# Kernel tuning notes

Measured on AMD Instinct MI355X. Metric: run time of the kernel, lower is better.

Reference implementation:

```python
import jax, jax.numpy as jnp
import numpy as np

N_NODES = 50000

def _gcn_layer(x, src, dst, W, b, n_nodes):
    # Linear transform first (PyG GCNConv): h = x @ W
    h = x @ W  # [N, out]
    # Add self-loops
    loop = jnp.arange(n_nodes, dtype=src.dtype)
    src2 = jnp.concatenate([src, loop])
    dst2 = jnp.concatenate([dst, loop])
    # Symmetric normalization deg^-1/2 (deg counts incoming edges incl. self-loop)
    deg = jax.ops.segment_sum(jnp.ones_like(dst2, dtype=h.dtype), dst2, num_segments=n_nodes)
    dinv = jnp.where(deg > 0, jax.lax.rsqrt(deg), 0.0)
    norm = dinv[src2] * dinv[dst2]  # [E+N]
    # Gather-scale-scatter aggregation
    msg = h[src2] * norm[:, None]  # [E+N, out]
    out = jax.ops.segment_sum(msg, dst2, num_segments=n_nodes)
    return out + b

def setup_inputs() -> dict:
    key = jax.random.key(0)
    k1, k2, k3, k4 = jax.random.split(key, 4)
    E = 800000
    x = jax.random.normal(k1, (N_NODES, 128), dtype=jnp.float32)
    edge_index = jax.random.randint(k2, (2, E), 0, N_NODES, dtype=jnp.int64)
    W1 = jax.random.normal(k3, (128, 512), dtype=jnp.float32) * (1.0 / np.sqrt(128))
    b1 = jnp.zeros((512,), dtype=jnp.float32)
    W2 = jax.random.normal(k4, (512, 250), dtype=jnp.float32) * (1.0 / np.sqrt(512))
    b2 = jnp.zeros((250,), dtype=jnp.float32)
    return {"x": x, "edge_index": edge_index, "W1": W1, "b1": b1, "W2": W2, "b2": b2}

def reference(x, edge_index, W1, b1, W2, b2):
    src, dst = edge_index[0], edge_index[1]
    h = _gcn_layer(x, src, dst, W1, b1, N_NODES)
    h = jax.nn.relu(h)
    h = _gcn_layer(h, src, dst, W2, b2, N_NODES)
    return jax.nn.relu(h)
```

## Files before the change

### kernel.cpp

```cpp
#include <hip/hip_runtime.h>

#define N_NODES 50000

typedef __attribute__((ext_vector_type(8))) short bf16x8;
typedef __attribute__((ext_vector_type(4))) float f32x4;

__device__ __forceinline__ ushort f2bf(float f) {
    union { float f; unsigned u; } v; v.f = f;
    unsigned r = v.u + 0x7fff + ((v.u >> 16) & 1);
    return (ushort)(r >> 16);
}
__device__ __forceinline__ float bf2f(ushort u) {
    union { unsigned u; float f; } v; v.u = ((unsigned)u) << 16;
    return v.f;
}
__device__ __forceinline__ float bf2f_lo(unsigned u) {
    union { unsigned u; float f; } v; v.u = u << 16;
    return v.f;
}
__device__ __forceinline__ float bf2f_hi(unsigned u) {
    union { unsigned u; float f; } v; v.u = u & 0xffff0000u;
    return v.f;
}

__device__ __forceinline__ int eload(const void* ei, int idx, int is64) {
    return is64 ? (int)((const long long*)ei)[idx] : ((const int*)ei)[idx];
}

__global__ void k_init(const void* ei, int* flag, int* deg, int n) {
    if (blockIdx.x == 0) {
        __shared__ int bad;
        if (threadIdx.x == 0) bad = 0;
        __syncthreads();
        long long v = ((const long long*)ei)[threadIdx.x];
        if (v < 0 || v >= N_NODES) atomicOr(&bad, 1);
        __syncthreads();
        if (threadIdx.x == 0) *flag = bad ? 0 : 1;
    }
    int i = blockIdx.x * 256 + threadIdx.x;
    if (i < n) deg[i] = 0;
}

__global__ void k_hist(const void* ei, const int* flag, int* deg, int e) {
    int base = (blockIdx.x * blockDim.x + threadIdx.x) * 4;
    if (base >= e) return;
    int is64 = *flag;
    if (base + 4 <= e) {
        int d0 = eload(ei, e + base,     is64);
        int d1 = eload(ei, e + base + 1, is64);
        int d2 = eload(ei, e + base + 2, is64);
        int d3 = eload(ei, e + base + 3, is64);
        atomicAdd(&deg[d0], 1);
        atomicAdd(&deg[d1], 1);
        atomicAdd(&deg[d2], 1);
        atomicAdd(&deg[d3], 1);
    } else {
        for (int i = base; i < e; ++i)
            atomicAdd(&deg[eload(ei, e + i, is64)], 1);
    }
}

__global__ __launch_bounds__(512)
void k_scanA(const int* __restrict__ deg, int* __restrict__ rp1,
             int* __restrict__ bsum, int n) {
    __shared__ int wsum[8];
    const int i = blockIdx.x * 512 + threadIdx.x;
    const int lane = threadIdx.x & 63, wid = threadIdx.x >> 6;
    int x = (i < n) ? deg[i] : 0;
    #pragma unroll
    for (int off = 1; off < 64; off <<= 1) {
        int y = __shfl_up(x, off, 64);
        if (lane >= off) x += y;
    }
    if (lane == 63) wsum[wid] = x;
    __syncthreads();
    if (wid == 0 && lane < 8) {
        int s = wsum[lane];
        #pragma unroll
        for (int off = 1; off < 8; off <<= 1) {
            int y = __shfl_up(s, off, 64);
            if (lane >= off) s += y;
        }
        wsum[lane] = s;
    }
    __syncthreads();
    int incl = x + (wid > 0 ? wsum[wid - 1] : 0);
    if (i < n) rp1[i] = incl;
    if (threadIdx.x == 0) bsum[blockIdx.x] = wsum[7];
}

__global__ __launch_bounds__(512)
void k_scanC(const int* __restrict__ deg, int* __restrict__ rowptr,
             const int* __restrict__ bsum, int* __restrict__ cur,
             float* __restrict__ dinv, int n, int nb) {
    __shared__ int spart[2];
    if (threadIdx.x < 128) {
        int v = (threadIdx.x < nb && (int)threadIdx.x < (int)blockIdx.x)
                ? bsum[threadIdx.x] : 0;
        #pragma unroll
        for (int o = 32; o; o >>= 1) v += __shfl_down(v, o, 64);
        if ((threadIdx.x & 63) == 0) spart[threadIdx.x >> 6] = v;
    }
    __syncthreads();
    const int off = spart[0] + spart[1];
    const int i = blockIdx.x * 512 + threadIdx.x;
    if (i >= n) return;
    const int d = deg[i];
    const int incl = rowptr[i + 1] + off;
    rowptr[i + 1] = incl;
    cur[i] = incl - d;
    dinv[i] = rsqrtf((float)(d + 1));
    if (i == 0) rowptr[0] = 0;
}

__global__ void k_fill(const void* ei, const int* flag, int* cur, int* adj, int e) {
    const int phase = blockIdx.x & 7;
    const int lo = phase * (N_NODES / 8);
    const int hi = lo + (N_NODES / 8);
    const int i = (blockIdx.x >> 3) * 256 + threadIdx.x;
    if (i >= e) return;
    const int is64 = *flag;
    const int d = eload(ei, e + i, is64);
    if (d >= lo && d < hi) {
        const int s = eload(ei, i, is64);
        adj[atomicAdd(&cur[d], 1)] = s;
    }
}

__global__ void k_splitW(const float* __restrict__ W1, const float* __restrict__ W2,
                         ushort* __restrict__ o1, ushort* __restrict__ o2) {
    int idx = blockIdx.x * 256 + threadIdx.x;
    if (idx < 512 * 128) {
        int nn = idx >> 7, k = idx & 127;
        o1[idx] = f2bf(W1[(size_t)k * 512 + nn]);
    } else {
        idx -= 512 * 128;
        int nn = idx >> 9, k = idx & 511;
        o2[idx] = (nn < 250) ? f2bf(W2[(size_t)k * 250 + nn]) : (ushort)0;
    }
}

__global__ __launch_bounds__(256)
void k_scale(const float* __restrict__ x, const float* __restrict__ dinv,
             ushort* __restrict__ xs, int n) {
    int idx = blockIdx.x * 256 + threadIdx.x;
    if (idx >= n * 64) return;
    int i = idx >> 6;
    float2 v = ((const float2*)x)[idx];
    float d = dinv[i];
    ((unsigned*)xs)[idx] = (unsigned)f2bf(d * v.x) | ((unsigned)f2bf(d * v.y) << 16);
}

__global__ __launch_bounds__(256)
void k_pull128b(const int* __restrict__ rowptr, const int* __restrict__ adj,
                const float* __restrict__ dinv, const ushort* __restrict__ xs,
                ushort* __restrict__ ohi, int n) {
    const int i = blockIdx.x * 4 + (threadIdx.x >> 6);
    if (i >= n) return;
    const int lane = threadIdx.x & 63;
    const unsigned* xs32 = (const unsigned*)xs;
    unsigned u = xs32[(size_t)i * 64 + lane];
    float a0 = bf2f_lo(u), a1 = bf2f_hi(u);
    int j = rowptr[i];
    const int end = rowptr[i + 1];
    for (; j + 8 <= end; j += 8) {
        int s0 = adj[j],     s1 = adj[j + 1], s2 = adj[j + 2], s3 = adj[j + 3];
        int s4 = adj[j + 4], s5 = adj[j + 5], s6 = adj[j + 6], s7 = adj[j + 7];
        unsigned u0 = xs32[(size_t)s0 * 64 + lane];
        unsigned u1 = xs32[(size_t)s1 * 64 + lane];
        unsigned u2 = xs32[(size_t)s2 * 64 + lane];
        unsigned u3 = xs32[(size_t)s3 * 64 + lane];
        unsigned u4 = xs32[(size_t)s4 * 64 + lane];
        unsigned u5 = xs32[(size_t)s5 * 64 + lane];
        unsigned u6 = xs32[(size_t)s6 * 64 + lane];
        unsigned u7 = xs32[(size_t)s7 * 64 + lane];
        a0 += bf2f_lo(u0) + bf2f_lo(u1) + bf2f_lo(u2) + bf2f_lo(u3);
        a1 += bf2f_hi(u0) + bf2f_hi(u1) + bf2f_hi(u2) + bf2f_hi(u3);
        a0 += bf2f_lo(u4) + bf2f_lo(u5) + bf2f_lo(u6) + bf2f_lo(u7);
        a1 += bf2f_hi(u4) + bf2f_hi(u5) + bf2f_hi(u6) + bf2f_hi(u7);
    }
    for (; j + 4 <= end; j += 4) {
        int s0 = adj[j], s1 = adj[j + 1], s2 = adj[j + 2], s3 = adj[j + 3];
        unsigned u0 = xs32[(size_t)s0 * 64 + lane];
        unsigned u1 = xs32[(size_t)s1 * 64 + lane];
        unsigned u2 = xs32[(size_t)s2 * 64 + lane];
        unsigned u3 = xs32[(size_t)s3 * 64 + lane];
        a0 += bf2f_lo(u0) + bf2f_lo(u1) + bf2f_lo(u2) + bf2f_lo(u3);
        a1 += bf2f_hi(u0) + bf2f_hi(u1) + bf2f_hi(u2) + bf2f_hi(u3);
    }
    for (; j < end; ++j) {
        unsigned us = xs32[(size_t)adj[j] * 64 + lane];
        a0 += bf2f_lo(us);
        a1 += bf2f_hi(us);
    }
    const float di = dinv[i];
    a0 *= di; a1 *= di;
    ((unsigned*)ohi)[(size_t)i * 64 + lane] =
        (unsigned)f2bf(a0) | ((unsigned)f2bf(a1) << 16);
}

__global__ __launch_bounds__(256)
void k_pull250v(const int* __restrict__ rowptr, const int* __restrict__ adj,
                const float* __restrict__ dinv, const ushort* __restrict__ t,
                const float* __restrict__ bias, float* __restrict__ out, int n) {
    const int i = blockIdx.x * 4 + (threadIdx.x >> 6);
    if (i >= n) return;
    const int lane = threadIdx.x & 63;
    const uint2* t2 = (const uint2*)t;
    uint2 u = t2[(size_t)i * 64 + lane];
    float a0 = bf2f_lo(u.x), a1 = bf2f_hi(u.x);
    float a2 = bf2f_lo(u.y), a3 = bf2f_hi(u.y);
    int j = rowptr[i];
    const int end = rowptr[i + 1];
    for (; j + 8 <= end; j += 8) {
        int s0 = adj[j],     s1 = adj[j + 1], s2 = adj[j + 2], s3 = adj[j + 3];
        int s4 = adj[j + 4], s5 = adj[j + 5], s6 = adj[j + 6], s7 = adj[j + 7];
        uint2 u0 = t2[(size_t)s0 * 64 + lane];
        uint2 u1 = t2[(size_t)s1 * 64 + lane];
        uint2 u2 = t2[(size_t)s2 * 64 + lane];
        uint2 u3 = t2[(size_t)s3 * 64 + lane];
        uint2 u4 = t2[(size_t)s4 * 64 + lane];
        uint2 u5 = t2[(size_t)s5 * 64 + lane];
        uint2 u6 = t2[(size_t)s6 * 64 + lane];
        uint2 u7 = t2[(size_t)s7 * 64 + lane];
        a0 += bf2f_lo(u0.x) + bf2f_lo(u1.x) + bf2f_lo(u2.x) + bf2f_lo(u3.x);
        a1 += bf2f_hi(u0.x) + bf2f_hi(u1.x) + bf2f_hi(u2.x) + bf2f_hi(u3.x);
        a2 += bf2f_lo(u0.y) + bf2f_lo(u1.y) + bf2f_lo(u2.y) + bf2f_lo(u3.y);
        a3 += bf2f_hi(u0.y) + bf2f_hi(u1.y) + bf2f_hi(u2.y) + bf2f_hi(u3.y);
        a0 += bf2f_lo(u4.x) + bf2f_lo(u5.x) + bf2f_lo(u6.x) + bf2f_lo(u7.x);
        a1 += bf2f_hi(u4.x) + bf2f_hi(u5.x) + bf2f_hi(u6.x) + bf2f_hi(u7.x);
        a2 += bf2f_lo(u4.y) + bf2f_lo(u5.y) + bf2f_lo(u6.y) + bf2f_lo(u7.y);
        a3 += bf2f_hi(u4.y) + bf2f_hi(u5.y) + bf2f_hi(u6.y) + bf2f_hi(u7.y);
    }
    for (; j + 4 <= end; j += 4) {
        int s0 = adj[j], s1 = adj[j + 1], s2 = adj[j + 2], s3 = adj[j + 3];
        uint2 u0 = t2[(size_t)s0 * 64 + lane];
        uint2 u1 = t2[(size_t)s1 * 64 + lane];
        uint2 u2 = t2[(size_t)s2 * 64 + lane];
        uint2 u3 = t2[(size_t)s3 * 64 + lane];
        a0 += bf2f_lo(u0.x) + bf2f_lo(u1.x) + bf2f_lo(u2.x) + bf2f_lo(u3.x);
        a1 += bf2f_hi(u0.x) + bf2f_hi(u1.x) + bf2f_hi(u2.x) + bf2f_hi(u3.x);
        a2 += bf2f_lo(u0.y) + bf2f_lo(u1.y) + bf2f_lo(u2.y) + bf2f_lo(u3.y);
        a3 += bf2f_hi(u0.y) + bf2f_hi(u1.y) + bf2f_hi(u2.y) + bf2f_hi(u3.y);
    }
    for (; j < end; ++j) {
        uint2 us = t2[(size_t)adj[j] * 64 + lane];
        a0 += bf2f_lo(us.x); a1 += bf2f_hi(us.x);
        a2 += bf2f_lo(us.y); a3 += bf2f_hi(us.y);
    }
    const float d = dinv[i];
    const int c0 = lane * 4;
    if (lane < 62) {
        float2 b0 = *(const float2*)&bias[c0];
        float2 b1 = *(const float2*)&bias[c0 + 2];
        float2 o0, o1;
        o0.x = fmaxf(d * a0 + b0.x, 0.0f);
        o0.y = fmaxf(d * a1 + b0.y, 0.0f);
        o1.x = fmaxf(d * a2 + b1.x, 0.0f);
        o1.y = fmaxf(d * a3 + b1.y, 0.0f);
        *(float2*)&out[(size_t)i * 250 + c0] = o0;
        *(float2*)&out[(size_t)i * 250 + c0 + 2] = o1;
    } else if (lane == 62) {
        float2 b0 = *(const float2*)&bias[248];
        float2 o0;
        o0.x = fmaxf(d * a0 + b0.x, 0.0f);
        o0.y = fmaxf(d * a1 + b0.y, 0.0f);
        *(float2*)&out[(size_t)i * 250 + 248] = o0;
    }
}

__device__ __forceinline__ void gl16(const ushort* g, ushort* l) {
    __builtin_amdgcn_global_load_lds((const __attribute__((address_space(1))) void*)g,
                                     (__attribute__((address_space(3))) void*)l,
                                     16, 0, 0);
}

#define OFF_B 4096
#define SMEM_HALF 12288

__global__ __launch_bounds__(256, 2)
void k_mfma(const ushort* __restrict__ A, const ushort* __restrict__ B,
            const float* __restrict__ bias, const float* __restrict__ rscale,
            ushort* __restrict__ outp, int M, int K, int ldc, int mode,
            int CX, int PY) {
    __shared__ __align__(16) ushort smem[2 * SMEM_HALF];

    int id = blockIdx.x;
    const int gsz = CX * 8;
    const int nfull = (PY >> 3) * gsz;
    int bx, by;
    if (id < nfull) {
        int gg = id / gsz;
        int r  = id - gg * gsz;
        bx = r >> 3;
        by = gg * 8 + (r & 7);
    } else {
        int rem  = id - nfull;
        int pbase = (PY >> 3) << 3;
        int prem  = PY - pbase;
        by = pbase + rem % prem;
        bx = rem / prem;
    }
    const int brow = by * 128;
    const int bcol = bx * 256;

    const int tid  = threadIdx.x;
    const int lane = tid & 63;
    const int w    = tid >> 6;
    const int g    = lane >> 4;
    const int lr   = lane & 15;

    auto STAGE = [&](ushort* buf, int k0) {
        const int kofs = k0 + w * 8;
        #pragma unroll
        for (int t2 = 0; t2 < 2; ++t2)
            gl16(A + (size_t)(brow + t2 * 64 + lane) * K + kofs,
                 buf + w * 1024 + t2 * 512);
        #pragma unroll
        for (int t4 = 0; t4 < 4; ++t4)
            gl16(B + (size_t)(bcol + t4 * 64 + lane) * K + kofs,
                 buf + OFF_B + w * 2048 + t4 * 512);
    };

    f32x4 acc[8][4] = {};

    auto COMPUTE = [&](const ushort* rb) {
        bf16x8 af[8], bh[4];
        #pragma unroll
        for (int nt = 0; nt < 4; ++nt)
            bh[nt] = *(const bf16x8*)(rb + OFF_B + g * 2048 + (w * 64 + nt * 16 + lr) * 8);
        #pragma unroll
        for (int mt = 0; mt < 8; ++mt)
            af[mt] = *(const bf16x8*)(rb + g * 1024 + (mt * 16 + lr) * 8);
        #pragma unroll
        for (int mt = 0; mt < 8; ++mt)
            #pragma unroll
            for (int nt = 0; nt < 4; ++nt)
                acc[mt][nt] = __builtin_amdgcn_mfma_f32_16x16x32_bf16(bh[nt], af[mt], acc[mt][nt], 0, 0, 0);
    };

    STAGE(smem, 0);
    int cur = 0;
    for (int k0 = 32; k0 < K; k0 += 32) {
        STAGE(smem + (cur ^ 1) * SMEM_HALF, k0);
        asm volatile("s_waitcnt vmcnt(6)" ::: "memory");
        __builtin_amdgcn_sched_barrier(0);
        __builtin_amdgcn_s_barrier();
        COMPUTE(smem + cur * SMEM_HALF);
        __builtin_amdgcn_sched_barrier(0);
        __builtin_amdgcn_s_barrier();
        cur ^= 1;
    }
    asm volatile("s_waitcnt vmcnt(0)" ::: "memory");
    __builtin_amdgcn_sched_barrier(0);
    __builtin_amdgcn_s_barrier();
    COMPUTE(smem + cur * SMEM_HALF);

    #pragma unroll
    for (int mt = 0; mt < 8; ++mt) {
        const int gr = brow + mt * 16 + lr;
        if (gr >= M) continue;
        const float rs = (mode == 0) ? rscale[gr] : 0.0f;
        #pragma unroll
        for (int nt = 0; nt < 4; ++nt) {
            const int gc0 = bcol + w * 64 + nt * 16 + g * 4;
            float v0, v1, v2, v3;
            if (mode == 0) {
                v0 = acc[mt][nt][0] * rs; v1 = acc[mt][nt][1] * rs;
                v2 = acc[mt][nt][2] * rs; v3 = acc[mt][nt][3] * rs;
            } else {
                const float4 bv = *(const float4*)&bias[gc0];
                v0 = fmaxf(acc[mt][nt][0] + bv.x, 0.0f);
                v1 = fmaxf(acc[mt][nt][1] + bv.y, 0.0f);
                v2 = fmaxf(acc[mt][nt][2] + bv.z, 0.0f);
                v3 = fmaxf(acc[mt][nt][3] + bv.w, 0.0f);
            }
            uint2 pk;
            pk.x = (unsigned)f2bf(v0) | ((unsigned)f2bf(v1) << 16);
            pk.y = (unsigned)f2bf(v2) | ((unsigned)f2bf(v3) << 16);
            *(uint2*)(outp + (size_t)gr * ldc + gc0) = pk;
        }
    }
}

extern "C" void kernel_launch(void* const* d_in, const int* in_sizes, int n_in,
                              void* d_out, int out_size, void* d_ws, size_t ws_size,
                              hipStream_t stream) {
    const float* x  = (const float*)d_in[0];
    const void*  ei = d_in[1];
    const float* W1 = (const float*)d_in[2];
    const float* b1 = (const float*)d_in[3];
    const float* W2 = (const float*)d_in[4];
    const float* b2 = (const float*)d_in[5];
    float* out = (float*)d_out;

    const int N = N_NODES;
    const int E = in_sizes[1] / 2;
    const int MPAD = 50048;
    const int NSCB = (N + 511) / 512;

    char* base = (char*)d_ws;
    int*   flag   = (int*)base;
    int*   deg    = (int*)(base + 256);
    int*   rowptr = deg + 51200;
    int*   cur    = rowptr + 51200;
    float* dinv   = (float*)(cur + 51200);
    int*   bsum   = (int*)(dinv + 51200);
    int*   adj    = bsum + 128;
    char*  p      = (char*)(adj + ((E + 63) & ~63));
    ushort* A1hi  = (ushort*)p;  p += (size_t)MPAD * 128 * 2;
    ushort* A1xx  = (ushort*)p;  p += (size_t)MPAD * 128 * 2;
    ushort* tbuf  = A1hi;
    ushort* h1hi  = (ushort*)p;  p += (size_t)MPAD * 512 * 2;
    ushort* Bt1   = (ushort*)p;  p += 512 * 128 * 2;
    ushort* Bt2   = (ushort*)p;  p += 256 * 512 * 2;
    ushort* xs    = (ushort*)p;  p += (size_t)MPAD * 128 * 2;
    (void)A1xx;

    k_init<<<(N + 255) / 256, 256, 0, stream>>>(ei, flag, deg, N);
    k_hist<<<(E / 4 + 255) / 256, 256, 0, stream>>>(ei, flag, deg, E);
    k_scanA<<<NSCB, 512, 0, stream>>>(deg, rowptr + 1, bsum, N);
    k_scanC<<<NSCB, 512, 0, stream>>>(deg, rowptr, bsum, cur, dinv, N, NSCB);
    k_fill<<<((E + 255) / 256) * 8, 256, 0, stream>>>(ei, flag, cur, adj, E);

    k_splitW<<<(512 * 128 + 256 * 512) / 256, 256, 0, stream>>>(W1, W2, Bt1, Bt2);
    k_scale<<<(N * 64 + 255) / 256, 256, 0, stream>>>(x, dinv, xs, N);

    k_pull128b<<<(N + 3) / 4, 256, 0, stream>>>(rowptr, adj, dinv, xs, A1hi, N);

    k_mfma<<<2 * 391, 256, 0, stream>>>(A1hi, Bt1, b1, nullptr, h1hi,
                                        N, 128, 512, 1, 2, 391);

    k_mfma<<<1 * 391, 256, 0, stream>>>(h1hi, Bt2, nullptr, dinv, tbuf,
                                        N, 512, 256, 0, 1, 391);

    k_pull250v<<<(N + 3) / 4, 256, 0, stream>>>(rowptr, adj, dinv, tbuf, b2, out, N);
}
```

Before: 264.4 us.

## Add dedicated single-shot K=128 GEMM kernel and fold weight conversion into init

Measured after the change: 264.8 us. About the same (+0.2%).

```diff
diff --git a/kernel.cpp b/kernel.cpp
--- a/kernel.cpp
+++ b/kernel.cpp
@@ -27,7 +27,9 @@
     return is64 ? (int)((const long long*)ei)[idx] : ((const int*)ei)[idx];
 }
 
-__global__ void k_init(const void* ei, int* flag, int* deg, int n) {
+__global__ void k_init(const void* ei, int* flag, int* deg, int n,
+                       const float* __restrict__ W1, const float* __restrict__ W2,
+                       ushort* __restrict__ o1, ushort* __restrict__ o2) {
     if (blockIdx.x == 0) {
         __shared__ int bad;
         if (threadIdx.x == 0) bad = 0;
@@ -39,6 +41,14 @@
     }
     int i = blockIdx.x * 256 + threadIdx.x;
     if (i < n) deg[i] = 0;
+    if (i < 512 * 128) {
+        int nn = i >> 7, k = i & 127;
+        o1[i] = f2bf(W1[(size_t)k * 512 + nn]);
+    } else if (i < 512 * 128 + 256 * 512) {
+        int idx = i - 512 * 128;
+        int nn = idx >> 9, k = idx & 511;
+        o2[idx] = (nn < 250) ? f2bf(W2[(size_t)k * 250 + nn]) : (ushort)0;
+    }
 }
 
 __global__ void k_hist(const void* ei, const int* flag, int* deg, int e) {
@@ -124,19 +134,6 @@
     if (d >= lo && d < hi) {
         const int s = eload(ei, i, is64);
         adj[atomicAdd(&cur[d], 1)] = s;
-    }
-}
-
-__global__ void k_splitW(const float* __restrict__ W1, const float* __restrict__ W2,
-                         ushort* __restrict__ o1, ushort* __restrict__ o2) {
-    int idx = blockIdx.x * 256 + threadIdx.x;
-    if (idx < 512 * 128) {
-        int nn = idx >> 7, k = idx & 127;
-        o1[idx] = f2bf(W1[(size_t)k * 512 + nn]);
-    } else {
-        idx -= 512 * 128;
-        int nn = idx >> 9, k = idx & 511;
-        o2[idx] = (nn < 250) ? f2bf(W2[(size_t)k * 250 + nn]) : (ushort)0;
     }
 }
 
@@ -275,15 +272,13 @@
                                      16, 0, 0);
 }
 
-#define OFF_B 4096
-#define SMEM_HALF 12288
+#define G1_OFFB 16384
 
 __global__ __launch_bounds__(256, 2)
-void k_mfma(const ushort* __restrict__ A, const ushort* __restrict__ B,
-            const float* __restrict__ bias, const float* __restrict__ rscale,
-            ushort* __restrict__ outp, int M, int K, int ldc, int mode,
-            int CX, int PY) {
-    __shared__ __align__(16) ushort smem[2 * SMEM_HALF];
+void k_mfma1(const ushort* __restrict__ A, const ushort* __restrict__ B,
+             const float* __restrict__ bias, ushort* __restrict__ outp,
+             int M, int CX, int PY) {
+    __shared__ __align__(16) ushort smem[32768];
 
     int id = blockIdx.x;
     const int gsz = CX * 8;
@@ -302,11 +297,94 @@
         bx = rem / prem;
     }
     const int brow = by * 128;
+    const int bcol = bx * 128;
+
+    const int lane = threadIdx.x & 63;
+    const int w    = threadIdx.x >> 6;
+    const int g    = lane >> 4;
+    const int lr   = lane & 15;
+    const int wm   = w >> 1, wn = w & 1;
+
+    #pragma unroll
+    for (int t = 0; t < 8; ++t) {
+        const int idx = w * 8 + t;
+        const int c  = idx >> 1;
+        const int r0 = (idx & 1) * 64;
+        const int doff = c * 1024 + r0 * 8;
+        gl16(A + (size_t)(brow + r0 + lane) * 128 + c * 8, smem + doff);
+        gl16(B + (size_t)(bcol + r0 + lane) * 128 + c * 8, smem + G1_OFFB + doff);
+    }
+    asm volatile("s_waitcnt vmcnt(0)" ::: "memory");
+    __builtin_amdgcn_sched_barrier(0);
+    __builtin_amdgcn_s_barrier();
+
+    f32x4 acc[4][4] = {};
+    #pragma unroll
+    for (int ks = 0; ks < 4; ++ks) {
+        bf16x8 af[4], bh[4];
+        const int cb = (ks * 4 + g) * 1024;
+        #pragma unroll
+        for (int i = 0; i < 4; ++i) {
+            af[i] = *(const bf16x8*)(smem + cb + (wm * 64 + i * 16 + lr) * 8);
+            bh[i] = *(const bf16x8*)(smem + G1_OFFB + cb + (wn * 64 + i * 16 + lr) * 8);
+        }
+        #pragma unroll
+        for (int mt = 0; mt < 4; ++mt)
+            #pragma unroll
+            for (int nt = 0; nt < 4; ++nt)
+                acc[mt][nt] = __builtin_amdgcn_mfma_f32_16x16x32_bf16(bh[nt], af[mt], acc[mt][nt], 0, 0, 0);
+    }
+
+    #pragma unroll
+    for (int mt = 0; mt < 4; ++mt) {
+        const int gr = brow + wm * 64 + mt * 16 + lr;
+        if (gr >= M) continue;
+        #pragma unroll
+        for (int nt = 0; nt < 4; ++nt) {
+            const int gc0 = bcol + wn * 64 + nt * 16 + g * 4;
+            const float4 bv = *(const float4*)&bias[gc0];
+            float v0 = fmaxf(acc[mt][nt][0] + bv.x, 0.0f);
+            float v1 = fmaxf(acc[mt][nt][1] + bv.y, 0.0f);
+            float v2 = fmaxf(acc[mt][nt][2] + bv.z, 0.0f);
+            float v3 = fmaxf(acc[mt][nt][3] + bv.w, 0.0f);
+            uint2 pk;
+            pk.x = (unsigned)f2bf(v0) | ((unsigned)f2bf(v1) << 16);
+            pk.y = (unsigned)f2bf(v2) | ((unsigned)f2bf(v3) << 16);
+            *(uint2*)(outp + (size_t)gr * 512 + gc0) = pk;
+        }
+    }
+}
+
+#define OFF_B 4096
+#define SMEM_HALF 12288
+
+__global__ __launch_bounds__(256, 2)
+void k_mfma(const ushort* __restrict__ A, const ushort* __restrict__ B,
+            const float* __restrict__ rscale, ushort* __restrict__ outp,
+            int M, int K, int ldc, int CX, int PY) {
+    __shared__ __align__(16) ushort smem[2 * SMEM_HALF];
+
+    int id = blockIdx.x;
+    const int gsz = CX * 8;
+    const int nfull = (PY >> 3) * gsz;
+    int bx, by;
+    if (id < nfull) {
+        int gg = id / gsz;
+        int r  = id - gg * gsz;
+        bx = r >> 3;
+        by = gg * 8 + (r & 7);
+    } else {
+        int rem  = id - nfull;
+        int pbase = (PY >> 3) << 3;
+        int prem  = PY - pbase;
+        by = pbase + rem % prem;
+        bx = rem / prem;
+    }
+    const int brow = by * 128;
     const int bcol = bx * 256;
 
-    const int tid  = threadIdx.x;
-    const int lane = tid & 63;
-    const int w    = tid >> 6;
+    const int lane = threadIdx.x & 63;
+    const int w    = threadIdx.x >> 6;
     const int g    = lane >> 4;
     const int lr   = lane & 15;
 
@@ -360,24 +438,15 @@
     for (int mt = 0; mt < 8; ++mt) {
         const int gr = brow + mt * 16 + lr;
         if (gr >= M) continue;
-        const float rs = (mode == 0) ? rscale[gr] : 0.0f;
+        const float rs = rscale[gr];
         #pragma unroll
         for (int nt = 0; nt < 4; ++nt) {
             const int gc0 = bcol + w * 64 + nt * 16 + g * 4;
-            float v0, v1, v2, v3;
-            if (mode == 0) {
-                v0 = acc[mt][nt][0] * rs; v1 = acc[mt][nt][1] * rs;
-                v2 = acc[mt][nt][2] * rs; v3 = acc[mt][nt][3] * rs;
-            } else {
-                const float4 bv = *(const float4*)&bias[gc0];
-                v0 = fmaxf(acc[mt][nt][0] + bv.x, 0.0f);
-                v1 = fmaxf(acc[mt][nt][1] + bv.y, 0.0f);
-                v2 = fmaxf(acc[mt][nt][2] + bv.z, 0.0f);
-                v3 = fmaxf(acc[mt][nt][3] + bv.w, 0.0f);
-            }
             uint2 pk;
-            pk.x = (unsigned)f2bf(v0) | ((unsigned)f2bf(v1) << 16);
-            pk.y = (unsigned)f2bf(v2) | ((unsigned)f2bf(v3) << 16);
+            pk.x = (unsigned)f2bf(acc[mt][nt][0] * rs) |
+                   ((unsigned)f2bf(acc[mt][nt][1] * rs) << 16);
+            pk.y = (unsigned)f2bf(acc[mt][nt][2] * rs) |
+                   ((unsigned)f2bf(acc[mt][nt][3] * rs) << 16);
             *(uint2*)(outp + (size_t)gr * ldc + gc0) = pk;
         }
     }
@@ -417,22 +486,20 @@
     ushort* xs    = (ushort*)p;  p += (size_t)MPAD * 128 * 2;
     (void)A1xx;
 
-    k_init<<<(N + 255) / 256, 256, 0, stream>>>(ei, flag, deg, N);
+    const int initBlocks = (512 * 128 + 256 * 512 + 255) / 256;
+    k_init<<<initBlocks, 256, 0, stream>>>(ei, flag, deg, N, W1, W2, Bt1, Bt2);
     k_hist<<<(E / 4 + 255) / 256, 256, 0, stream>>>(ei, flag, deg, E);
     k_scanA<<<NSCB, 512, 0, stream>>>(deg, rowptr + 1, bsum, N);
     k_scanC<<<NSCB, 512, 0, stream>>>(deg, rowptr, bsum, cur, dinv, N, NSCB);
     k_fill<<<((E + 255) / 256) * 8, 256, 0, stream>>>(ei, flag, cur, adj, E);
 
-    k_splitW<<<(512 * 128 + 256 * 512) / 256, 256, 0, stream>>>(W1, W2, Bt1, Bt2);
     k_scale<<<(N * 64 + 255) / 256, 256, 0, stream>>>(x, dinv, xs, N);
 
     k_pull128b<<<(N + 3) / 4, 256, 0, stream>>>(rowptr, adj, dinv, xs, A1hi, N);
 
-    k_mfma<<<2 * 391, 256, 0, stream>>>(A1hi, Bt1, b1, nullptr, h1hi,
-                                        N, 128, 512, 1, 2, 391);
-
-    k_mfma<<<1 * 391, 256, 0, stream>>>(h1hi, Bt2, nullptr, dinv, tbuf,
-                                        N, 512, 256, 0, 1, 391);
+    k_mfma1<<<4 * 391, 256, 0, stream>>>(A1hi, Bt1, b1, h1hi, N, 4, 391);
+
+    k_mfma<<<1 * 391, 256, 0, stream>>>(h1hi, Bt2, dinv, tbuf, N, 512, 256, 1, 391);
 
     k_pull250v<<<(N + 3) / 4, 256, 0, stream>>>(rowptr, adj, dinv, tbuf, b2, out, N);
 }
```
